# Performance work log

Hardware: AMD Instinct MI355X
Metric: run time of the kernel (lower is better)

The kernel has to match this reference:

```python
import jax, jax.numpy as jnp
import numpy as np

B, T, D = 2, 4096, 1024
H, DK, DV = 8, 128, 128   # head dims (expand_k = expand_v = 1.0)
INTER = 4096
CHUNK = 128
EPS = 1e-5


def rmsnorm(x, w, eps=EPS):
    return x * jax.lax.rsqrt(jnp.mean(x * x, axis=-1, keepdims=True) + eps) * w


def linear_attention(x, Wq, Wk, Wv, Wo, out_norm_w):
    # identity feature map, causal linear attention, per-head RMSNorm output norm
    b, t, d = x.shape
    n = t // CHUNK
    q = (x @ Wq).reshape(b, t, H, DK).transpose(0, 2, 1, 3)  # [B,H,T,DK]
    k = (x @ Wk).reshape(b, t, H, DK).transpose(0, 2, 1, 3)
    v = (x @ Wv).reshape(b, t, H, DV).transpose(0, 2, 1, 3)
    # chunked O(T * d^2) causal linear attention
    qc = q.reshape(b, H, n, CHUNK, DK).transpose(2, 0, 1, 3, 4)  # [N,B,H,C,DK]
    kc = k.reshape(b, H, n, CHUNK, DK).transpose(2, 0, 1, 3, 4)
    vc = v.reshape(b, H, n, CHUNK, DV).transpose(2, 0, 1, 3, 4)
    causal = jnp.tril(jnp.ones((CHUNK, CHUNK), dtype=bool))

    def step(S, qkv):
        qb, kb, vb = qkv  # each [B,H,C,d]
        attn = jnp.einsum('bhid,bhjd->bhij', qb, kb)
        attn = jnp.where(causal, attn, 0.0)
        o = jnp.einsum('bhij,bhjv->bhiv', attn, vb) + jnp.einsum('bhid,bhdv->bhiv', qb, S)
        S = S + jnp.einsum('bhid,bhiv->bhdv', kb, vb)
        return S, o

    S0 = jnp.zeros((b, H, DK, DV), x.dtype)
    _, o = jax.lax.scan(step, S0, (qc, kc, vc))      # o: [N,B,H,C,DV]
    o = o.transpose(1, 2, 0, 3, 4).reshape(b, H, t, DV)
    o = rmsnorm(o, out_norm_w)                        # per-head output RMSNorm
    o = o.transpose(0, 2, 1, 3).reshape(b, t, H * DV)
    return o @ Wo


def setup_inputs() -> dict:
    key = jax.random.key(0)
    ks = jax.random.split(key, 9)
    s = 0.02
    return {
        'hidden_states': jax.random.normal(ks[0], (B, T, D), jnp.float32),
        'attn_norm_w': jnp.ones((D,), jnp.float32),
        'Wq': jax.random.normal(ks[1], (D, H * DK), jnp.float32) * s,
        'Wk': jax.random.normal(ks[2], (D, H * DK), jnp.float32) * s,
        'Wv': jax.random.normal(ks[3], (D, H * DV), jnp.float32) * s,
        'Wo': jax.random.normal(ks[4], (H * DV, D), jnp.float32) * s,
        'attn_out_norm_w': jnp.ones((DV,), jnp.float32),
        'mlp_norm_w': jnp.ones((D,), jnp.float32),
        'Wgate': jax.random.normal(ks[5], (D, INTER), jnp.float32) * s,
        'Wup': jax.random.normal(ks[6], (D, INTER), jnp.float32) * s,
        'Wdown': jax.random.normal(ks[7], (INTER, D), jnp.float32) * s,
    }


def reference(hidden_states, attn_norm_w, Wq, Wk, Wv, Wo, attn_out_norm_w,
              mlp_norm_w, Wgate, Wup, Wdown):
    x = hidden_states
    # attn sub-block: RMSNorm -> linear attention -> residual
    h = rmsnorm(x, attn_norm_w)
    x = x + linear_attention(h, Wq, Wk, Wv, Wo, attn_out_norm_w)
    # mlp sub-block: RMSNorm -> SwiGLU -> residual
    h = rmsnorm(x, mlp_norm_w)
    x = x + (jax.nn.silu(h @ Wgate) * (h @ Wup)) @ Wdown
    return x
```

## Files before the change

### kernel.cpp

```cpp
#include <hip/hip_runtime.h>
#include <hip/hip_bf16.h>
#include <stdint.h>


typedef __hip_bfloat16 bf16;
typedef __bf16 bf16x8 __attribute__((ext_vector_type(8)));
typedef float f32x4 __attribute__((ext_vector_type(4)));

union Frag {
  uint4 u;
  bf16x8 b;
  unsigned short s[8];
};

__device__ __forceinline__ float bf2f(unsigned short v) {
  union { unsigned int u; float f; } c;
  c.u = (unsigned int)v << 16;
  return c.f;
}
__device__ __forceinline__ unsigned short f2bf(float f) {
  union { float f; unsigned int u; } c;
  c.f = f;
  unsigned int u = c.u;
  u += 0x7fffu + ((u >> 16) & 1u);
  return (unsigned short)(u >> 16);
}

__device__ __forceinline__ void gload16(const unsigned short* g, unsigned short* l) {
  __builtin_amdgcn_global_load_lds(
      (const __attribute__((address_space(1))) unsigned int*)g,
      (__attribute__((address_space(3))) unsigned int*)l, 16, 0, 0);
}

__global__ __launch_bounds__(256) void k_rmsnorm(const float* __restrict__ x,
                                                 const float* __restrict__ w,
                                                 bf16* __restrict__ out) {
  const int row = blockIdx.x;
  const int t = threadIdx.x;
  float4 v = reinterpret_cast<const float4*>(x + (size_t)row * 1024)[t];
  float ss = v.x * v.x + v.y * v.y + v.z * v.z + v.w * v.w;
#pragma unroll
  for (int o = 32; o > 0; o >>= 1) ss += __shfl_xor(ss, o, 64);
  __shared__ float red[4];
  if ((t & 63) == 0) red[t >> 6] = ss;
  __syncthreads();
  float tot = red[0] + red[1] + red[2] + red[3];
  float sc = rsqrtf(tot * (1.f / 1024.f) + 1e-5f);
  float4 wv = reinterpret_cast<const float4*>(w)[t];
  ushort4 o4;
  o4.x = f2bf(v.x * sc * wv.x);
  o4.y = f2bf(v.y * sc * wv.y);
  o4.z = f2bf(v.z * sc * wv.z);
  o4.w = f2bf(v.w * sc * wv.w);
  reinterpret_cast<ushort4*>(out + (size_t)row * 1024)[t] = o4;
}

struct TP4 {
  const float* s[4];
  bf16* d[4];
};
__global__ __launch_bounds__(256) void k_transpose_w4(TP4 p) {
  __shared__ float tile[32][33];
  const int z = blockIdx.z;
  const float* W = p.s[z];
  unsigned short* WTu = (unsigned short*)p.d[z];
  const int bx = blockIdx.x * 32;
  const int by = blockIdx.y * 32;
  const int tx = threadIdx.x, ty = threadIdx.y;
#pragma unroll
  for (int i = 0; i < 4; i++)
    tile[ty + i * 8][tx] = W[(size_t)(by + ty + i * 8) * 1024 + bx + tx];
  __syncthreads();
#pragma unroll
  for (int i = 0; i < 4; i++)
    WTu[(size_t)(bx + ty + i * 8) * 1024 + by + tx] = f2bf(tile[tx][ty + i * 8]);
}

__global__ __launch_bounds__(256) void k_transpose_w(const float* __restrict__ W,
                                                     bf16* __restrict__ WT,
                                                     int R, int C) {
  __shared__ float tile[32][33];
  const int bx = blockIdx.x * 32;
  const int by = blockIdx.y * 32;
  const int tx = threadIdx.x, ty = threadIdx.y;
#pragma unroll
  for (int i = 0; i < 4; i++)
    tile[ty + i * 8][tx] = W[(size_t)(by + ty + i * 8) * C + bx + tx];
  __syncthreads();
  unsigned short* WTu = (unsigned short*)WT;
#pragma unroll
  for (int i = 0; i < 4; i++)
    WTu[(size_t)(bx + ty + i * 8) * R + by + tx] = f2bf(tile[tx][ty + i * 8]);
}

__global__ __launch_bounds__(256) void k_transpose_wgu(const float* __restrict__ Wg,
                                                       const float* __restrict__ Wu,
                                                       bf16* __restrict__ WT) {
  __shared__ float tile[32][33];
  const int which = blockIdx.z;
  const float* W = which ? Wu : Wg;
  const int bx = blockIdx.x * 32;
  const int by = blockIdx.y * 32;
  const int tx = threadIdx.x, ty = threadIdx.y;
#pragma unroll
  for (int i = 0; i < 4; i++)
    tile[ty + i * 8][tx] = W[(size_t)(by + ty + i * 8) * 4096 + bx + tx];
  __syncthreads();
  unsigned short* WTu = (unsigned short*)WT;
#pragma unroll
  for (int i = 0; i < 4; i++) {
    const int c = bx + ty + i * 8;
    const int fr = ((c >> 7) << 8) + which * 128 + (c & 127);
    WTu[(size_t)fr * 1024 + by + tx] = f2bf(tile[tx][ty + i * 8]);
  }
}

template <int BM, int EPI>
__global__ __launch_bounds__(512, 2) void k_gemm256(const bf16* __restrict__ A, int lda,
                                                    const bf16* __restrict__ BT,
                                                    const float* __restrict__ res,
                                                    void* __restrict__ Cout,
                                                    int N, int K) {
  constexpr int MR = BM / 64;
  constexpr int ASZ = BM * 64;
  constexpr int AHALF = BM * 32;
  constexpr int SLOTSZ = ASZ + 16384;
  __shared__ __align__(16) unsigned short lds[2 * SLOTSZ];

  const int gx = gridDim.x;
  const int nwg = gx * gridDim.y;
  const int lin = blockIdx.y * gx + blockIdx.x;
  const int swz = (lin & 7) * (nwg >> 3) + (lin >> 3);
  const int bm = (swz / gx) * BM, bn = (swz % gx) * 256;

  const int t = threadIdx.x;
  const int wid = t >> 6, lane = t & 63;
  const int wr = wid >> 2, wc = wid & 3;
  const int lm = lane & 15, kg = lane >> 4;
  const int x0 = ((kg ^ (lm & 7)) << 3);
  const int x1 = (((4 + kg) ^ (lm & 7)) << 3);
  const int scolS = (((lane & 7) ^ ((lane >> 3) & 7)) << 3);

  const unsigned short* Ab = (const unsigned short*)A;
  const unsigned short* Bb = (const unsigned short*)BT;

  auto stA = [&](int slot, int h, int tt) {
    if constexpr (BM == 256) {
      const unsigned short* g = Ab + (size_t)(bm + h * 64 + wid * 8 + (lane >> 3)) * lda +
                                (size_t)tt * 64 + scolS;
      unsigned short* d = &lds[slot * SLOTSZ + h * 8192 + wid * 512];
      gload16(g, d);
      gload16(g + (size_t)128 * lda, d + 4096);
    } else {
      const int i0 = wid * 8 + (lane >> 3);
      const unsigned short* g = Ab +
          (size_t)(bm + ((i0 >> 5) << 6) + h * 32 + (i0 & 31)) * lda +
          (size_t)tt * 64 + scolS;
      gload16(g, &lds[slot * SLOTSZ + h * 4096 + wid * 512]);
    }
  };
  auto stB = [&](int slot, int h, int tt) {
    const int i0 = wid * 8 + (lane >> 3);
    const unsigned short* g = Bb +
        (size_t)(bn + ((i0 >> 5) << 6) + h * 32 + (i0 & 31)) * K +
        (size_t)tt * 64 + scolS;
    unsigned short* d = &lds[slot * SLOTSZ + ASZ + h * 8192 + wid * 512];
    gload16(g, d);
    gload16(g + (size_t)128 * K, d + 4096);
  };
  auto vmn = [&]() {
    if constexpr (BM == 256) asm volatile("s_waitcnt vmcnt(8)" ::: "memory");
    else                     asm volatile("s_waitcnt vmcnt(6)" ::: "memory");
  };
  auto vm0 = [&]() { asm volatile("s_waitcnt vmcnt(0)" ::: "memory"); };

  f32x4 acc[2 * MR][4] = {};
  Frag af[MR][2], bf0[2][2], bf1[2][2];

#define LOADA(SLOT, MH)                                                        \
  {                                                                            \
    const int abase = (SLOT)*SLOTSZ + (MH)*AHALF + wr * (AHALF / 2) + lm * 64; \
    _Pragma("unroll") for (int m = 0; m < MR; m++) {                           \
      af[m][0].u = *(const uint4*)&lds[abase + m * 1024 + x0];                 \
      af[m][1].u = *(const uint4*)&lds[abase + m * 1024 + x1];                 \
    }                                                                          \
  }
#define LOADB(SLOT, NH, BF)                                                    \
  {                                                                            \
    const int bbase = (SLOT)*SLOTSZ + ASZ + (NH)*8192 + wc * 2048 + lm * 64;   \
    _Pragma("unroll") for (int n = 0; n < 2; n++) {                            \
      BF[n][0].u = *(const uint4*)&lds[bbase + n * 1024 + x0];                 \
      BF[n][1].u = *(const uint4*)&lds[bbase + n * 1024 + x1];                 \
    }                                                                          \
  }
#define PH(LOADS, STAGES, VMW, MH, NH, BF)                                     \
  {                                                                            \
    LOADS;                                                                     \
    STAGES;                                                                    \
    VMW;                                                                       \
    __builtin_amdgcn_s_setprio(1);                                             \
    _Pragma("unroll") for (int m = 0; m < MR; m++)                             \
    _Pragma("unroll") for (int n = 0; n < 2; n++) {                            \
      f32x4& ac = acc[(MH)*MR + m][(NH)*2 + n];                                \
      ac = __builtin_amdgcn_mfma_f32_16x16x32_bf16(af[m][0].b, BF[n][0].b, ac, 0, 0, 0); \
      ac = __builtin_amdgcn_mfma_f32_16x16x32_bf16(af[m][1].b, BF[n][1].b, ac, 0, 0, 0); \
    }                                                                          \
    __builtin_amdgcn_s_setprio(0);                                             \
    __builtin_amdgcn_s_barrier();                                              \
  }

  stA(0, 0, 0); stB(0, 0, 0); stB(0, 1, 0); stA(0, 1, 0);
  stA(1, 0, 1); stB(1, 0, 1); stB(1, 1, 1); stA(1, 1, 1);
  vmn();
  __builtin_amdgcn_s_barrier();

  const int NI = K / 128;
  for (int i = 0; i < NI; i++) {
    const int u = 2 * i;
    const bool st = (i + 1 < NI);
    PH(LOADA(0, 0); LOADB(0, 0, bf0), , , 0, 0, bf0)
    PH(LOADB(0, 1, bf1), { if (st) { stA(0, 0, u + 2); stB(0, 0, u + 2); } }, , 0, 1, bf1)
    PH(LOADA(0, 1), { if (st) stB(0, 1, u + 2); }, , 1, 0, bf0)
    PH(, { if (st) stA(0, 1, u + 2); }, if (st) { vmn(); } else { vm0(); }, 1, 1, bf1)
    PH(LOADA(1, 0); LOADB(1, 0, bf0), , , 0, 0, bf0)
    PH(LOADB(1, 1, bf1), { if (st) { stA(1, 0, u + 3); stB(1, 0, u + 3); } }, , 0, 1, bf1)
    PH(LOADA(1, 1), { if (st) stB(1, 1, u + 3); }, , 1, 0, bf0)
    PH(, { if (st) stA(1, 1, u + 3); }, if (st) { vmn(); }, 1, 1, bf1)
  }
#undef PH
#undef LOADA
#undef LOADB

  if constexpr (EPI == 1) {
    constexpr int PR = BM / 2;
    float* fl = (float*)lds;
    float* Co = (float*)Cout;
#pragma unroll
    for (int p = 0; p < 2; p++) {
      if (wr == p) {
#pragma unroll
        for (int m = 0; m < 2 * MR; m++)
#pragma unroll
          for (int n = 0; n < 4; n++)
#pragma unroll
            for (int r = 0; r < 4; r++)
              fl[(m * 16 + kg * 4 + r) * 256 + wc * 64 + n * 16 + lm] = acc[m][n][r];
      }
      __syncthreads();
#pragma unroll
      for (int j = 0; j < PR / 8; j++) {
        const int idx = t + j * 512;
        const int row = idx >> 6, seg = idx & 63;
        const size_t o = (size_t)(bm + p * PR + row) * N + bn + seg * 4;
        float4 v = *(const float4*)&fl[row * 256 + seg * 4];
        float4 rv = *(const float4*)&res[o];
        v.x += rv.x; v.y += rv.y; v.z += rv.z; v.w += rv.w;
        *(float4*)&Co[o] = v;
      }
      __syncthreads();
    }
  } else {
#pragma unroll
    for (int m = 0; m < 2 * MR; m++)
#pragma unroll
      for (int n = 0; n < 4; n++)
#pragma unroll
        for (int r = 0; r < 4; r++)
          lds[(wr * (BM / 2) + m * 16 + kg * 4 + r) * 256 + wc * 64 + n * 16 + lm] =
              f2bf(acc[m][n][r]);
    __syncthreads();
    unsigned short* Cu = (unsigned short*)Cout;
    if constexpr (EPI == 0) {
#pragma unroll
      for (int j = 0; j < BM / 16; j++) {
        const int idx = t + j * 512;
        const int row = idx >> 5, seg = idx & 31;
        *(uint4*)(Cu + (size_t)(bm + row) * N + bn + seg * 8) =
            *(const uint4*)&lds[row * 256 + seg * 8];
      }
    } else {
      const int No = N >> 1;
#pragma unroll
      for (int j = 0; j < BM / 32; j++) {
        const int idx = t + j * 512;
        const int row = idx >> 4, seg = idx & 15;
        Frag gf, uf, rr;
        gf.u = *(const uint4*)&lds[row * 256 + seg * 8];
        uf.u = *(const uint4*)&lds[row * 256 + 128 + seg * 8];
#pragma unroll
        for (int a = 0; a < 8; a++) {
          float g = bf2f(gf.s[a]);
          float uu = bf2f(uf.s[a]);
          rr.s[a] = f2bf(g / (1.f + __expf(-g)) * uu);
        }
        *(uint4*)(Cu + (size_t)(bm + row) * No + (bn >> 1) + seg * 8) = rr.u;
      }
    }
  }
}

__global__ __launch_bounds__(256) void k_chunk_kv(const bf16* __restrict__ qkv,
                                                  float* __restrict__ G,
                                                  bf16* __restrict__ VT) {
  __shared__ __align__(16) unsigned short ks[128][128];
  __shared__ __align__(16) unsigned short vs[128][136];
  const int idx = blockIdx.x;
  const int cc = idx & 31, bh = idx >> 5, bb = bh >> 3, hh = bh & 7;
  const unsigned short* qkvu = (const unsigned short*)qkv;
  const unsigned short* kp = qkvu + (size_t)(bb * 4096 + cc * 128) * 3072 + 1024 + hh * 128;
  const unsigned short* vp = kp + 1024;
  const int t = threadIdx.x;
#pragma unroll
  for (int i = 0; i < 8; i++) {
    int ch = t + i * 256;
    int r = ch >> 4, c8 = (ch & 15) << 3;
    *(uint4*)&ks[r][c8] = *(const uint4*)(kp + (size_t)r * 3072 + c8);
    *(uint4*)&vs[r][c8] = *(const uint4*)(vp + (size_t)r * 3072 + c8);
  }
  __syncthreads();
  const int dv0 = (t >> 4) * 8, dk0 = (t & 15) * 8;
  float acc[8][8] = {};
  for (int j = 0; j < 128; j++) {
    Frag kf, vf;
    vf.u = *(const uint4*)&vs[j][dv0];
    kf.u = *(const uint4*)&ks[j][dk0];
    float kx[8], vx[8];
#pragma unroll
    for (int a = 0; a < 8; a++) { kx[a] = bf2f(kf.s[a]); vx[a] = bf2f(vf.s[a]); }
#pragma unroll
    for (int a = 0; a < 8; a++)
#pragma unroll
      for (int b2 = 0; b2 < 8; b2++) acc[a][b2] += vx[a] * kx[b2];
  }
  float* Gp = G + (size_t)idx * 16384;
#pragma unroll
  for (int a = 0; a < 8; a++)
#pragma unroll
    for (int b2 = 0; b2 < 8; b2 += 4) {
      float4 w4 = make_float4(acc[a][b2], acc[a][b2 + 1], acc[a][b2 + 2], acc[a][b2 + 3]);
      *(float4*)(Gp + (size_t)(dv0 + a) * 128 + dk0 + b2) = w4;
    }
  unsigned short* vo = (unsigned short*)VT + (size_t)bh * 524288 + cc * 128;
#pragma unroll
  for (int i = 0; i < 8; i++) {
    const int dv = (t >> 4) + i * 16;
    const int r0 = (t & 15) * 8;
    Frag f;
#pragma unroll
    for (int j = 0; j < 8; j++) f.s[j] = vs[r0 + j][dv];
    *(uint4*)(vo + (size_t)dv * 4096 + r0) = f.u;
  }
}

__global__ __launch_bounds__(256) void k_prefix(const float* __restrict__ G,
                                                bf16* __restrict__ S) {
  const size_t gid = (size_t)blockIdx.x * 256 + threadIdx.x;
  const size_t bh = gid >> 14, e = gid & 16383;
  const float* gp = G + (bh << 5) * 16384 + e;
  unsigned short* sp = (unsigned short*)S + (bh << 5) * 16384 + e;
  float run = 0.f;
  for (int c2 = 0; c2 < 32; c2++) {
    sp[(size_t)c2 << 14] = f2bf(run);
    run += gp[(size_t)c2 << 14];
  }
}

__global__ __launch_bounds__(256) void k_attn2(const bf16* __restrict__ qkv,
                                               const bf16* __restrict__ VT,
                                               const bf16* __restrict__ ST,
                                               const float* __restrict__ nw,
                                               bf16* __restrict__ A2) {
  __shared__ __align__(16) unsigned short Qs[128][136];
  __shared__ __align__(16) unsigned short Ks[128][136];
  __shared__ __align__(16) unsigned short Bs[128][136];
  __shared__ float red[128][2];

  const int idx = blockIdx.x;
  const int cc = idx & 31, bh = idx >> 5, bb = bh >> 3, hh = bh & 7;
  const size_t rowbase = (size_t)(bb * 4096 + cc * 128);
  const unsigned short* qp = (const unsigned short*)qkv + rowbase * 3072 + hh * 128;
  const unsigned short* kp = qp + 1024;
  const unsigned short* vtp = (const unsigned short*)VT + (size_t)bh * 524288 + cc * 128;
  const unsigned short* stp = (const unsigned short*)ST + ((size_t)idx << 14);

  const int t = threadIdx.x;
  const int wid = t >> 6, lane = t & 63;
  const int wm = (wid >> 1) * 64, wn = (wid & 1) * 64;
  const int lm = lane & 15, kg = lane >> 4;
  const int sr = t >> 4;
  const int sc = (t & 15) << 3;

#pragma unroll
  for (int i = 0; i < 8; i++) {
    int r = sr + i * 16;
    *(uint4*)&Qs[r][sc] = *(const uint4*)(qp + (size_t)r * 3072 + sc);
    *(uint4*)&Ks[r][sc] = *(const uint4*)(kp + (size_t)r * 3072 + sc);
    *(uint4*)&Bs[r][sc] = *(const uint4*)(vtp + (size_t)r * 4096 + sc);
  }
  __syncthreads();

  f32x4 acc[4][4] = {};
#pragma unroll
  for (int kk = 0; kk < 4; kk++) {
    Frag af[4], bfr[4];
#pragma unroll
    for (int i = 0; i < 4; i++) {
      af[i].u = *(const uint4*)&Qs[wm + i * 16 + lm][kk * 32 + kg * 8];
      bfr[i].u = *(const uint4*)&Ks[wn + i * 16 + lm][kk * 32 + kg * 8];
    }
#pragma unroll
    for (int mi = 0; mi < 4; mi++)
#pragma unroll
      for (int ni = 0; ni < 4; ni++)
        acc[mi][ni] = __builtin_amdgcn_mfma_f32_16x16x32_bf16(af[mi].b, bfr[ni].b,
                                                              acc[mi][ni], 0, 0, 0);
  }
  __syncthreads();

#pragma unroll
  for (int mi = 0; mi < 4; mi++)
#pragma unroll
    for (int r = 0; r < 4; r++) {
      const int gi = wm + mi * 16 + kg * 4 + r;
#pragma unroll
      for (int ni = 0; ni < 4; ni++) {
        const int gj = wn + ni * 16 + lm;
        Ks[gi][gj] = f2bf(gj <= gi ? acc[mi][ni][r] : 0.f);
      }
    }
  __syncthreads();

  f32x4 oa[4][4] = {};
#pragma unroll
  for (int kk = 0; kk < 4; kk++) {
    Frag af[4], bfr[4];
#pragma unroll
    for (int i = 0; i < 4; i++) {
      af[i].u = *(const uint4*)&Ks[wm + i * 16 + lm][kk * 32 + kg * 8];
      bfr[i].u = *(const uint4*)&Bs[wn + i * 16 + lm][kk * 32 + kg * 8];
    }
#pragma unroll
    for (int mi = 0; mi < 4; mi++)
#pragma unroll
      for (int ni = 0; ni < 4; ni++)
        oa[mi][ni] = __builtin_amdgcn_mfma_f32_16x16x32_bf16(af[mi].b, bfr[ni].b,
                                                             oa[mi][ni], 0, 0, 0);
  }
  __syncthreads();

#pragma unroll
  for (int i = 0; i < 8; i++) {
    int r = sr + i * 16;
    *(uint4*)&Bs[r][sc] = *(const uint4*)(stp + (size_t)r * 128 + sc);
  }
  __syncthreads();

#pragma unroll
  for (int kk = 0; kk < 4; kk++) {
    Frag af[4], bfr[4];
#pragma unroll
    for (int i = 0; i < 4; i++) {
      af[i].u = *(const uint4*)&Qs[wm + i * 16 + lm][kk * 32 + kg * 8];
      bfr[i].u = *(const uint4*)&Bs[wn + i * 16 + lm][kk * 32 + kg * 8];
    }
#pragma unroll
    for (int mi = 0; mi < 4; mi++)
#pragma unroll
      for (int ni = 0; ni < 4; ni++)
        oa[mi][ni] = __builtin_amdgcn_mfma_f32_16x16x32_bf16(af[mi].b, bfr[ni].b,
                                                             oa[mi][ni], 0, 0, 0);
  }

#pragma unroll
  for (int mi = 0; mi < 4; mi++)
#pragma unroll
    for (int r = 0; r < 4; r++) {
      float ss = 0.f;
#pragma unroll
      for (int ni = 0; ni < 4; ni++) ss += oa[mi][ni][r] * oa[mi][ni][r];
      ss += __shfl_xor(ss, 1, 64);
      ss += __shfl_xor(ss, 2, 64);
      ss += __shfl_xor(ss, 4, 64);
      ss += __shfl_xor(ss, 8, 64);
      if (lm == 0) red[wm + mi * 16 + kg * 4 + r][wid & 1] = ss;
    }
  __syncthreads();

#pragma unroll
  for (int mi = 0; mi < 4; mi++)
#pragma unroll
    for (int r = 0; r < 4; r++) {
      const int gi = wm + mi * 16 + kg * 4 + r;
      const float tot = red[gi][0] + red[gi][1];
      const float scl = rsqrtf(tot * (1.f / 128.f) + 1e-5f);
#pragma unroll
      for (int ni = 0; ni < 4; ni++) {
        const int gj = wn + ni * 16 + lm;
        Ks[gi][gj] = f2bf(oa[mi][ni][r] * scl * nw[gj]);
      }
    }
  __syncthreads();

  unsigned short* A2u = (unsigned short*)A2;
#pragma unroll
  for (int i = 0; i < 8; i++) {
    int r = sr + i * 16;
    *(uint4*)(A2u + (rowbase + r) * 1024 + hh * 128 + sc) = *(const uint4*)&Ks[r][sc];
  }
}

extern "C" void kernel_launch(void* const* d_in, const int* in_sizes, int n_in,
                              void* d_out, int out_size, void* d_ws, size_t ws_size,
                              hipStream_t stream) {
  const float* x = (const float*)d_in[0];
  const float* anw = (const float*)d_in[1];
  const float* Wq = (const float*)d_in[2];
  const float* Wk = (const float*)d_in[3];
  const float* Wv = (const float*)d_in[4];
  const float* Wo = (const float*)d_in[5];
  const float* onw = (const float*)d_in[6];
  const float* mnw = (const float*)d_in[7];
  const float* Wg = (const float*)d_in[8];
  const float* Wu = (const float*)d_in[9];
  const float* Wd = (const float*)d_in[10];
  float* out = (float*)d_out;

  char* base = (char*)d_ws;
  size_t off = 0;
  auto alloc = [&](size_t bytes) -> char* {
    char* q = base + off;
    off += (bytes + 255) & ~(size_t)255;
    return q;
  };
  bf16* WqkvT = (bf16*)alloc(3072ll * 1024 * 2);
  bf16* WoT   = (bf16*)alloc(1024ll * 1024 * 2);
  bf16* WguT  = (bf16*)alloc(8192ll * 1024 * 2);
  bf16* WdT   = (bf16*)alloc(1024ll * 4096 * 2);
  bf16* h     = (bf16*)alloc(8192ll * 1024 * 2);
  float* x1   = (float*)alloc(8192ll * 1024 * 4);
  char* pool  = alloc(8192ll * 3072 * 2 + 16ll * 32 * 16384 * 4 +
                      16ll * 32 * 16384 * 2 + 16ll * 128 * 4096 * 2);
  bf16* qkv = (bf16*)pool;
  float* G  = (float*)(pool + 8192ll * 3072 * 2);
  bf16* S   = (bf16*)(pool + 8192ll * 3072 * 2 + 16ll * 32 * 16384 * 4);
  bf16* VT  = (bf16*)(pool + 8192ll * 3072 * 2 + 16ll * 32 * 16384 * 4 +
                      16ll * 32 * 16384 * 2);
  bf16* act = (bf16*)pool;

  const dim3 tb32(32, 8);
  TP4 tp;
  tp.s[0] = Wq; tp.d[0] = WqkvT;
  tp.s[1] = Wk; tp.d[1] = WqkvT + 1024ll * 1024;
  tp.s[2] = Wv; tp.d[2] = WqkvT + 2048ll * 1024;
  tp.s[3] = Wo; tp.d[3] = WoT;
  k_transpose_w4<<<dim3(32, 32, 4), tb32, 0, stream>>>(tp);
  k_transpose_wgu<<<dim3(128, 32, 2), tb32, 0, stream>>>(Wg, Wu, WguT);
  k_transpose_w<<<dim3(32, 128), tb32, 0, stream>>>(Wd, WdT, 4096, 1024);

  k_rmsnorm<<<8192, 256, 0, stream>>>(x, anw, h);
  k_gemm256<128, 0><<<dim3(12, 64), 512, 0, stream>>>(h, 1024, WqkvT, nullptr, qkv, 3072, 1024);
  k_chunk_kv<<<512, 256, 0, stream>>>(qkv, G, VT);
  k_prefix<<<1024, 256, 0, stream>>>(G, S);
  k_attn2<<<512, 256, 0, stream>>>(qkv, VT, S, onw, h);
  k_gemm256<128, 1><<<dim3(4, 64), 512, 0, stream>>>(h, 1024, WoT, x, x1, 1024, 1024);

  k_rmsnorm<<<8192, 256, 0, stream>>>(x1, mnw, h);
  k_gemm256<256, 3><<<dim3(32, 32), 512, 0, stream>>>(h, 1024, WguT, nullptr, act, 8192, 1024);
  k_gemm256<128, 1><<<dim3(4, 64), 512, 0, stream>>>(act, 4096, WdT, x1, out, 1024, 4096);
}
```

Baseline: 463.4 us.

## Replace 256-wide 8-wave GEMM with simpler 128x128 4-wave double-buffered GEMM

Replaces the templated 256-column, 512-thread GEMM with its eight-phase interleaved pipeline by a 128x128-tile, 256-thread kernel. The new kernel does a plain two-slot double-buffered loop: each iteration loads fragments, stages the tile after next, then runs all MFMAs. The gate/up weight interleave changes from 128-column to 64-column groups to match the narrower tile, and all launch grids double. The aim is more workgroups and better occupancy. In exchange it gives up operand reuse per tile and the finer overlap of loads and MFMAs.

```diff
diff --git a/kernel.cpp b/kernel.cpp
--- a/kernel.cpp
+++ b/kernel.cpp
@@ -110,190 +110,158 @@
 #pragma unroll
   for (int i = 0; i < 4; i++) {
     const int c = bx + ty + i * 8;
-    const int fr = ((c >> 7) << 8) + which * 128 + (c & 127);
+    const int fr = ((c >> 6) << 7) + which * 64 + (c & 63);
     WTu[(size_t)fr * 1024 + by + tx] = f2bf(tile[tx][ty + i * 8]);
   }
 }
 
-template <int BM, int EPI>
-__global__ __launch_bounds__(512, 2) void k_gemm256(const bf16* __restrict__ A, int lda,
+template <int EPI>
+__global__ __launch_bounds__(256, 2) void k_gemm128(const bf16* __restrict__ A, int lda,
                                                     const bf16* __restrict__ BT,
                                                     const float* __restrict__ res,
                                                     void* __restrict__ Cout,
                                                     int N, int K) {
-  constexpr int MR = BM / 64;
-  constexpr int ASZ = BM * 64;
-  constexpr int AHALF = BM * 32;
-  constexpr int SLOTSZ = ASZ + 16384;
+  constexpr int SLOTSZ = 16384;
   __shared__ __align__(16) unsigned short lds[2 * SLOTSZ];
 
   const int gx = gridDim.x;
   const int nwg = gx * gridDim.y;
   const int lin = blockIdx.y * gx + blockIdx.x;
   const int swz = (lin & 7) * (nwg >> 3) + (lin >> 3);
-  const int bm = (swz / gx) * BM, bn = (swz % gx) * 256;
+  const int bm = (swz / gx) * 128, bn = (swz % gx) * 128;
 
   const int t = threadIdx.x;
   const int wid = t >> 6, lane = t & 63;
-  const int wr = wid >> 2, wc = wid & 3;
+  const int wr = wid >> 1, wc = wid & 1;
   const int lm = lane & 15, kg = lane >> 4;
   const int x0 = ((kg ^ (lm & 7)) << 3);
   const int x1 = (((4 + kg) ^ (lm & 7)) << 3);
-  const int scolS = (((lane & 7) ^ ((lane >> 3) & 7)) << 3);
+  const int srow = t >> 3;
+  const int scolS = (((t & 7) ^ (srow & 7)) << 3);
 
   const unsigned short* Ab = (const unsigned short*)A;
   const unsigned short* Bb = (const unsigned short*)BT;
 
-  auto stA = [&](int slot, int h, int tt) {
-    if constexpr (BM == 256) {
-      const unsigned short* g = Ab + (size_t)(bm + h * 64 + wid * 8 + (lane >> 3)) * lda +
-                                (size_t)tt * 64 + scolS;
-      unsigned short* d = &lds[slot * SLOTSZ + h * 8192 + wid * 512];
-      gload16(g, d);
-      gload16(g + (size_t)128 * lda, d + 4096);
+  auto stage = [&](int s, int tt) {
+#pragma unroll
+    for (int g = 0; g < 4; g++)
+      gload16(Ab + (size_t)(bm + g * 32 + srow) * lda + (size_t)tt * 64 + scolS,
+              &lds[s * SLOTSZ + g * 2048 + wid * 512]);
+#pragma unroll
+    for (int g = 0; g < 4; g++)
+      gload16(Bb + (size_t)(bn + g * 32 + srow) * K + (size_t)tt * 64 + scolS,
+              &lds[s * SLOTSZ + 8192 + g * 2048 + wid * 512]);
+  };
+
+  f32x4 acc[4][4] = {};
+  Frag af[4][2], bf[4][2];
+
+  const int NT = K / 64;
+  stage(0, 0);
+  stage(1, 1);
+  asm volatile("s_waitcnt vmcnt(8)" ::: "memory");
+  __builtin_amdgcn_s_barrier();
+
+  for (int i = 0; i < NT; i++) {
+    const int s = i & 1;
+    const int ab = s * SLOTSZ;
+#pragma unroll
+    for (int m = 0; m < 4; m++) {
+      const int r = (wr * 64 + m * 16 + lm) * 64;
+      af[m][0].u = *(const uint4*)&lds[ab + r + x0];
+      af[m][1].u = *(const uint4*)&lds[ab + r + x1];
+    }
+#pragma unroll
+    for (int n = 0; n < 4; n++) {
+      const int r = 8192 + (wc * 64 + n * 16 + lm) * 64;
+      bf[n][0].u = *(const uint4*)&lds[ab + r + x0];
+      bf[n][1].u = *(const uint4*)&lds[ab + r + x1];
+    }
+    asm volatile("s_waitcnt lgkmcnt(0)" ::: "memory");
+    __builtin_amdgcn_s_barrier();
+    if (i + 2 < NT) {
+      stage(s, i + 2);
+      asm volatile("s_waitcnt vmcnt(8)" ::: "memory");
     } else {
-      const int i0 = wid * 8 + (lane >> 3);
-      const unsigned short* g = Ab +
-          (size_t)(bm + ((i0 >> 5) << 6) + h * 32 + (i0 & 31)) * lda +
-          (size_t)tt * 64 + scolS;
-      gload16(g, &lds[slot * SLOTSZ + h * 4096 + wid * 512]);
-    }
-  };
-  auto stB = [&](int slot, int h, int tt) {
-    const int i0 = wid * 8 + (lane >> 3);
-    const unsigned short* g = Bb +
-        (size_t)(bn + ((i0 >> 5) << 6) + h * 32 + (i0 & 31)) * K +
-        (size_t)tt * 64 + scolS;
-    unsigned short* d = &lds[slot * SLOTSZ + ASZ + h * 8192 + wid * 512];
-    gload16(g, d);
-    gload16(g + (size_t)128 * K, d + 4096);
-  };
-  auto vmn = [&]() {
-    if constexpr (BM == 256) asm volatile("s_waitcnt vmcnt(8)" ::: "memory");
-    else                     asm volatile("s_waitcnt vmcnt(6)" ::: "memory");
-  };
-  auto vm0 = [&]() { asm volatile("s_waitcnt vmcnt(0)" ::: "memory"); };
-
-  f32x4 acc[2 * MR][4] = {};
-  Frag af[MR][2], bf0[2][2], bf1[2][2];
-
-#define LOADA(SLOT, MH)                                                        \
-  {                                                                            \
-    const int abase = (SLOT)*SLOTSZ + (MH)*AHALF + wr * (AHALF / 2) + lm * 64; \
-    _Pragma("unroll") for (int m = 0; m < MR; m++) {                           \
-      af[m][0].u = *(const uint4*)&lds[abase + m * 1024 + x0];                 \
-      af[m][1].u = *(const uint4*)&lds[abase + m * 1024 + x1];                 \
-    }                                                                          \
-  }
-#define LOADB(SLOT, NH, BF)                                                    \
-  {                                                                            \
-    const int bbase = (SLOT)*SLOTSZ + ASZ + (NH)*8192 + wc * 2048 + lm * 64;   \
-    _Pragma("unroll") for (int n = 0; n < 2; n++) {                            \
-      BF[n][0].u = *(const uint4*)&lds[bbase + n * 1024 + x0];                 \
-      BF[n][1].u = *(const uint4*)&lds[bbase + n * 1024 + x1];                 \
-    }                                                                          \
-  }
-#define PH(LOADS, STAGES, VMW, MH, NH, BF)                                     \
-  {                                                                            \
-    LOADS;                                                                     \
-    STAGES;                                                                    \
-    VMW;                                                                       \
-    __builtin_amdgcn_s_setprio(1);                                             \
-    _Pragma("unroll") for (int m = 0; m < MR; m++)                             \
-    _Pragma("unroll") for (int n = 0; n < 2; n++) {                            \
-      f32x4& ac = acc[(MH)*MR + m][(NH)*2 + n];                                \
-      ac = __builtin_amdgcn_mfma_f32_16x16x32_bf16(af[m][0].b, BF[n][0].b, ac, 0, 0, 0); \
-      ac = __builtin_amdgcn_mfma_f32_16x16x32_bf16(af[m][1].b, BF[n][1].b, ac, 0, 0, 0); \
-    }                                                                          \
-    __builtin_amdgcn_s_setprio(0);                                             \
-    __builtin_amdgcn_s_barrier();                                              \
-  }
-
-  stA(0, 0, 0); stB(0, 0, 0); stB(0, 1, 0); stA(0, 1, 0);
-  stA(1, 0, 1); stB(1, 0, 1); stB(1, 1, 1); stA(1, 1, 1);
-  vmn();
-  __builtin_amdgcn_s_barrier();
-
-  const int NI = K / 128;
-  for (int i = 0; i < NI; i++) {
-    const int u = 2 * i;
-    const bool st = (i + 1 < NI);
-    PH(LOADA(0, 0); LOADB(0, 0, bf0), , , 0, 0, bf0)
-    PH(LOADB(0, 1, bf1), { if (st) { stA(0, 0, u + 2); stB(0, 0, u + 2); } }, , 0, 1, bf1)
-    PH(LOADA(0, 1), { if (st) stB(0, 1, u + 2); }, , 1, 0, bf0)
-    PH(, { if (st) stA(0, 1, u + 2); }, if (st) { vmn(); } else { vm0(); }, 1, 1, bf1)
-    PH(LOADA(1, 0); LOADB(1, 0, bf0), , , 0, 0, bf0)
-    PH(LOADB(1, 1, bf1), { if (st) { stA(1, 0, u + 3); stB(1, 0, u + 3); } }, , 0, 1, bf1)
-    PH(LOADA(1, 1), { if (st) stB(1, 1, u + 3); }, , 1, 0, bf0)
-    PH(, { if (st) stA(1, 1, u + 3); }, if (st) { vmn(); }, 1, 1, bf1)
-  }
-#undef PH
-#undef LOADA
-#undef LOADB
+      asm volatile("s_waitcnt vmcnt(0)" ::: "memory");
+    }
+    __builtin_amdgcn_s_barrier();
+    __builtin_amdgcn_s_setprio(1);
+#pragma unroll
+    for (int m = 0; m < 4; m++)
+#pragma unroll
+      for (int n = 0; n < 4; n++) {
+        acc[m][n] = __builtin_amdgcn_mfma_f32_16x16x32_bf16(af[m][0].b, bf[n][0].b,
+                                                            acc[m][n], 0, 0, 0);
+        acc[m][n] = __builtin_amdgcn_mfma_f32_16x16x32_bf16(af[m][1].b, bf[n][1].b,
+                                                            acc[m][n], 0, 0, 0);
+      }
+    __builtin_amdgcn_s_setprio(0);
+  }
 
   if constexpr (EPI == 1) {
-    constexpr int PR = BM / 2;
     float* fl = (float*)lds;
     float* Co = (float*)Cout;
 #pragma unroll
     for (int p = 0; p < 2; p++) {
+      __syncthreads();
       if (wr == p) {
 #pragma unroll
-        for (int m = 0; m < 2 * MR; m++)
+        for (int m = 0; m < 4; m++)
 #pragma unroll
           for (int n = 0; n < 4; n++)
 #pragma unroll
             for (int r = 0; r < 4; r++)
-              fl[(m * 16 + kg * 4 + r) * 256 + wc * 64 + n * 16 + lm] = acc[m][n][r];
+              fl[(m * 16 + kg * 4 + r) * 128 + wc * 64 + n * 16 + lm] = acc[m][n][r];
       }
       __syncthreads();
 #pragma unroll
-      for (int j = 0; j < PR / 8; j++) {
-        const int idx = t + j * 512;
-        const int row = idx >> 6, seg = idx & 63;
-        const size_t o = (size_t)(bm + p * PR + row) * N + bn + seg * 4;
-        float4 v = *(const float4*)&fl[row * 256 + seg * 4];
+      for (int j = 0; j < 8; j++) {
+        const int idx = t + j * 256;
+        const int row = idx >> 5, c4 = (idx & 31) << 2;
+        const size_t o = (size_t)(bm + p * 64 + row) * N + bn + c4;
+        float4 v = *(const float4*)&fl[row * 128 + c4];
         float4 rv = *(const float4*)&res[o];
         v.x += rv.x; v.y += rv.y; v.z += rv.z; v.w += rv.w;
         *(float4*)&Co[o] = v;
       }
-      __syncthreads();
     }
   } else {
-#pragma unroll
-    for (int m = 0; m < 2 * MR; m++)
+    __syncthreads();
+#pragma unroll
+    for (int m = 0; m < 4; m++)
 #pragma unroll
       for (int n = 0; n < 4; n++)
 #pragma unroll
         for (int r = 0; r < 4; r++)
-          lds[(wr * (BM / 2) + m * 16 + kg * 4 + r) * 256 + wc * 64 + n * 16 + lm] =
+          lds[(wr * 64 + m * 16 + kg * 4 + r) * 128 + wc * 64 + n * 16 + lm] =
               f2bf(acc[m][n][r]);
     __syncthreads();
     unsigned short* Cu = (unsigned short*)Cout;
     if constexpr (EPI == 0) {
 #pragma unroll
-      for (int j = 0; j < BM / 16; j++) {
-        const int idx = t + j * 512;
-        const int row = idx >> 5, seg = idx & 31;
+      for (int j = 0; j < 8; j++) {
+        const int idx = t + j * 256;
+        const int row = idx >> 4, seg = idx & 15;
         *(uint4*)(Cu + (size_t)(bm + row) * N + bn + seg * 8) =
-            *(const uint4*)&lds[row * 256 + seg * 8];
+            *(const uint4*)&lds[row * 128 + seg * 8];
       }
     } else {
       const int No = N >> 1;
 #pragma unroll
-      for (int j = 0; j < BM / 32; j++) {
-        const int idx = t + j * 512;
-        const int row = idx >> 4, seg = idx & 15;
+      for (int j = 0; j < 4; j++) {
+        const int idx = t + j * 256;
+        const int row = idx >> 3, s8 = (idx & 7) << 3;
         Frag gf, uf, rr;
-        gf.u = *(const uint4*)&lds[row * 256 + seg * 8];
-        uf.u = *(const uint4*)&lds[row * 256 + 128 + seg * 8];
+        gf.u = *(const uint4*)&lds[row * 128 + s8];
+        uf.u = *(const uint4*)&lds[row * 128 + 64 + s8];
 #pragma unroll
         for (int a = 0; a < 8; a++) {
           float g = bf2f(gf.s[a]);
           float uu = bf2f(uf.s[a]);
           rr.s[a] = f2bf(g / (1.f + __expf(-g)) * uu);
         }
-        *(uint4*)(Cu + (size_t)(bm + row) * No + (bn >> 1) + seg * 8) = rr.u;
+        *(uint4*)(Cu + (size_t)(bm + row) * No + (bn >> 1) + s8) = rr.u;
       }
     }
   }
@@ -558,13 +526,13 @@
   k_transpose_w<<<dim3(32, 128), tb32, 0, stream>>>(Wd, WdT, 4096, 1024);
 
   k_rmsnorm<<<8192, 256, 0, stream>>>(x, anw, h);
-  k_gemm256<128, 0><<<dim3(12, 64), 512, 0, stream>>>(h, 1024, WqkvT, nullptr, qkv, 3072, 1024);
+  k_gemm128<0><<<dim3(24, 64), 256, 0, stream>>>(h, 1024, WqkvT, nullptr, qkv, 3072, 1024);
   k_chunk_kv<<<512, 256, 0, stream>>>(qkv, G, VT);
   k_prefix<<<1024, 256, 0, stream>>>(G, S);
   k_attn2<<<512, 256, 0, stream>>>(qkv, VT, S, onw, h);
-  k_gemm256<128, 1><<<dim3(4, 64), 512, 0, stream>>>(h, 1024, WoT, x, x1, 1024, 1024);
+  k_gemm128<1><<<dim3(8, 64), 256, 0, stream>>>(h, 1024, WoT, x, x1, 1024, 1024);
 
   k_rmsnorm<<<8192, 256, 0, stream>>>(x1, mnw, h);
-  k_gemm256<256, 3><<<dim3(32, 32), 512, 0, stream>>>(h, 1024, WguT, nullptr, act, 8192, 1024);
-  k_gemm256<128, 1><<<dim3(4, 64), 512, 0, stream>>>(act, 4096, WdT, x1, out, 1024, 4096);
-}
+  k_gemm128<3><<<dim3(64, 64), 256, 0, stream>>>(h, 1024, WguT, nullptr, act, 8192, 1024);
+  k_gemm128<1><<<dim3(8, 64), 256, 0, stream>>>(act, 4096, WdT, x1, out, 1024, 4096);
+}
```

After: 464.7 us. No clear change (+0.3%).
